# Performance work log

Measured on AMD Instinct MI355X. Metric: run time of the kernel, lower is better.

The kernel has to match this reference:

```python
import jax, jax.numpy as jnp
import numpy as np

B, N, F_IN, F_OUT = 65536, 17, 64, 64


def setup_inputs() -> dict:
    key = jax.random.key(0)
    k1, k2, k3, k4 = jax.random.split(key, 4)
    x = jax.random.normal(k1, (B, N, F_IN), dtype=jnp.float32)
    adj = jax.random.uniform(k2, (N, N), dtype=jnp.float32)
    # symmetric 0/1-ish skeleton adjacency with self structure kept dense as in the module
    adj = (adj + adj.T) * 0.5
    weight_self = jax.random.normal(k3, (F_IN, F_OUT), dtype=jnp.float32) * (1.0 / np.sqrt(F_IN))
    weight_neighbor = jax.random.normal(k4, (F_IN, F_OUT), dtype=jnp.float32) * (1.0 / np.sqrt(F_IN))
    bias = jnp.zeros((F_OUT,), dtype=jnp.float32)
    return {"x": x, "adj": adj, "weight_self": weight_self,
            "weight_neighbor": weight_neighbor, "bias": bias}


def reference(x, adj, weight_self, weight_neighbor, bias):
    # out_self[b,n,o] = x[b,n,i] * W_self[i,o]
    out_self = jnp.einsum('bni,io->bno', x, weight_self)
    # neighbor aggregation: adj[n,m] * x[b,m,i]
    x_neighbors = jnp.einsum('nm,bmi->bni', adj, x)
    out_neighbors = jnp.einsum('bni,io->bno', x_neighbors, weight_neighbor)
    return out_self + out_neighbors + bias
```

## Files before the change

kernel.cpp:

```cpp
#include <hip/hip_runtime.h>
#include <stdint.h>

#define NNODE  17
#define FDIM   64
#define NBLOCK 512
#define GPW    32
#define SROW   68
#define WSTR   132

typedef __attribute__((ext_vector_type(4)))  short short4v;
typedef __attribute__((ext_vector_type(8)))  short short8v;
typedef __attribute__((ext_vector_type(16))) float f32x16;

__device__ __forceinline__ uint32_t bf16b(float f) {
    uint32_t u = __float_as_uint(f);
    return (u + 0x7fffu + ((u >> 16) & 1u)) >> 16;
}
__device__ __forceinline__ uint32_t bfpack(float lo, float hi) {
    return bf16b(lo) | (bf16b(hi) << 16);
}
__device__ __forceinline__ short8v ld8(const uint16_t* p) {
    short4v lo = *(const short4v*)p;
    short4v hi = *(const short4v*)(p + 4);
    return __builtin_shufflevector(lo, hi, 0, 1, 2, 3, 4, 5, 6, 7);
}
__device__ __forceinline__ short8v mk8(uint32_t w0, uint32_t w1, uint32_t w2, uint32_t w3) {
    union { uint32_t u[4]; short8v v; } c;
    c.u[0] = w0; c.u[1] = w1; c.u[2] = w2; c.u[3] = w3;
    return c.v;
}

__global__ __launch_bounds__(256, 2) void egc_kernel(
    const float* __restrict__ x, const float* __restrict__ adj,
    const float* __restrict__ wself, const float* __restrict__ wneigh,
    const float* __restrict__ bias, float* __restrict__ out)
{
    __shared__ uint16_t sMem[4 * 32 * SROW];
    __shared__ float sAdj[NNODE * NNODE];
    __shared__ float sBias[FDIM];

    const int t  = threadIdx.x;
    const int l  = t & 63;
    const int wv = t >> 6;
    const int n_ = l & 31;
    const int h_ = l >> 5;

    const int    gw    = blockIdx.x * 4 + wv;
    const size_t gbase = (size_t)gw * GPW;

    const float4* xg = (const float4*)x + gbase * 272;
    float4 pf0, pf1, pf2, pf3, pf4;
    pf0 = xg[l]; pf1 = xg[l + 64]; pf2 = xg[l + 128]; pf3 = xg[l + 192];
    if (l < 16) pf4 = xg[256 + l];

    for (int idx = t; idx < FDIM * 128; idx += 256) {
        int o = idx >> 7, k = idx & 127;
        float v = (k < 64) ? wself[k * 64 + o] : wneigh[(k - 64) * 64 + o];
        sMem[o * WSTR + k] = (uint16_t)bf16b(v);
    }
    for (int i = t; i < NNODE * NNODE; i += 256) sAdj[i] = adj[i];
    if (t < FDIM) sBias[t] = bias[t];
    __syncthreads();

    short8v wS[2][4], wN[2][4];
    #pragma unroll
    for (int nt = 0; nt < 2; ++nt)
        #pragma unroll
        for (int ks = 0; ks < 4; ++ks) {
            wS[nt][ks] = ld8(&sMem[(32 * nt + n_) * WSTR + 16 * ks + 8 * h_]);
            wN[nt][ks] = ld8(&sMem[(32 * nt + n_) * WSTR + 64 + 16 * ks + 8 * h_]);
        }
    const float bias0 = sBias[n_], bias1 = sBias[32 + n_];

    short8v adjA[2];
    #pragma unroll
    for (int ks = 0; ks < 2; ++ks) {
        short8v v;
        #pragma unroll
        for (int e = 0; e < 8; ++e) {
            int k = 16 * ks + 8 * h_ + e;
            float a = (n_ < NNODE && k < NNODE) ? sAdj[n_ * NNODE + k] : 0.f;
            v[e] = (short)bf16b(a);
        }
        adjA[ks] = v;
    }
    __syncthreads();
    for (int i = t; i < 4 * 32 * SROW; i += 256) sMem[i] = 0;
    __syncthreads();

    uint16_t* strip = &sMem[wv * 32 * SROW];
    float* outg = out + gbase * (size_t)(NNODE * FDIM);

    for (int g = 0; g < GPW; ++g) {
        {
            uint2 pk; int idx, row, c4;
            idx = l;       row = idx >> 4; c4 = (idx & 15) << 2;
            pk.x = bfpack(pf0.x, pf0.y); pk.y = bfpack(pf0.z, pf0.w);
            *(uint2*)&strip[row * SROW + c4] = pk;
            idx = l + 64;  row = idx >> 4; c4 = (idx & 15) << 2;
            pk.x = bfpack(pf1.x, pf1.y); pk.y = bfpack(pf1.z, pf1.w);
            *(uint2*)&strip[row * SROW + c4] = pk;
            idx = l + 128; row = idx >> 4; c4 = (idx & 15) << 2;
            pk.x = bfpack(pf2.x, pf2.y); pk.y = bfpack(pf2.z, pf2.w);
            *(uint2*)&strip[row * SROW + c4] = pk;
            idx = l + 192; row = idx >> 4; c4 = (idx & 15) << 2;
            pk.x = bfpack(pf3.x, pf3.y); pk.y = bfpack(pf3.z, pf3.w);
            *(uint2*)&strip[row * SROW + c4] = pk;
            if (l < 16) {
                pk.x = bfpack(pf4.x, pf4.y); pk.y = bfpack(pf4.z, pf4.w);
                *(uint2*)&strip[16 * SROW + (l << 2)] = pk;
            }
        }
        if (g + 1 < GPW) {
            xg += 272;
            pf0 = xg[l]; pf1 = xg[l + 64]; pf2 = xg[l + 128]; pf3 = xg[l + 192];
            if (l < 16) pf4 = xg[256 + l];
        }

        short8v a0 = ld8(&strip[n_ * SROW + 0  + 8 * h_]);
        short8v a1 = ld8(&strip[n_ * SROW + 16 + 8 * h_]);
        short8v a2 = ld8(&strip[n_ * SROW + 32 + 8 * h_]);
        short8v a3 = ld8(&strip[n_ * SROW + 48 + 8 * h_]);

        f32x16 s0, s1, h0, h1;
        #pragma unroll
        for (int r = 0; r < 16; ++r) { s0[r] = bias0; s1[r] = bias1; h0[r] = 0.f; h1[r] = 0.f; }

        s0 = __builtin_amdgcn_mfma_f32_32x32x16_bf16(a0, wS[0][0], s0, 0, 0, 0);
        s1 = __builtin_amdgcn_mfma_f32_32x32x16_bf16(a0, wS[1][0], s1, 0, 0, 0);
        h0 = __builtin_amdgcn_mfma_f32_32x32x16_bf16(a0, wN[0][0], h0, 0, 0, 0);
        h1 = __builtin_amdgcn_mfma_f32_32x32x16_bf16(a0, wN[1][0], h1, 0, 0, 0);
        s0 = __builtin_amdgcn_mfma_f32_32x32x16_bf16(a1, wS[0][1], s0, 0, 0, 0);
        s1 = __builtin_amdgcn_mfma_f32_32x32x16_bf16(a1, wS[1][1], s1, 0, 0, 0);
        h0 = __builtin_amdgcn_mfma_f32_32x32x16_bf16(a1, wN[0][1], h0, 0, 0, 0);
        h1 = __builtin_amdgcn_mfma_f32_32x32x16_bf16(a1, wN[1][1], h1, 0, 0, 0);
        s0 = __builtin_amdgcn_mfma_f32_32x32x16_bf16(a2, wS[0][2], s0, 0, 0, 0);
        s1 = __builtin_amdgcn_mfma_f32_32x32x16_bf16(a2, wS[1][2], s1, 0, 0, 0);
        h0 = __builtin_amdgcn_mfma_f32_32x32x16_bf16(a2, wN[0][2], h0, 0, 0, 0);
        h1 = __builtin_amdgcn_mfma_f32_32x32x16_bf16(a2, wN[1][2], h1, 0, 0, 0);
        s0 = __builtin_amdgcn_mfma_f32_32x32x16_bf16(a3, wS[0][3], s0, 0, 0, 0);
        s1 = __builtin_amdgcn_mfma_f32_32x32x16_bf16(a3, wS[1][3], s1, 0, 0, 0);
        h0 = __builtin_amdgcn_mfma_f32_32x32x16_bf16(a3, wN[0][3], h0, 0, 0, 0);
        h1 = __builtin_amdgcn_mfma_f32_32x32x16_bf16(a3, wN[1][3], h1, 0, 0, 0);

        #define HB_ADJ(SACC, HACC)                                                        \
        {                                                                                  \
            _Pragma("unroll")                                                              \
            for (int ks2 = 0; ks2 < 2; ++ks2) {                                            \
                const int rb = 8 * ks2;                                                    \
                float o0_ = __shfl_xor(h_ ? HACC[rb + 0] : HACC[rb + 4], 32);              \
                float o1_ = __shfl_xor(h_ ? HACC[rb + 1] : HACC[rb + 5], 32);              \
                float o2_ = __shfl_xor(h_ ? HACC[rb + 2] : HACC[rb + 6], 32);              \
                float o3_ = __shfl_xor(h_ ? HACC[rb + 3] : HACC[rb + 7], 32);              \
                uint32_t l01 = bfpack(HACC[rb + 0], HACC[rb + 1]);                         \
                uint32_t l23 = bfpack(HACC[rb + 2], HACC[rb + 3]);                         \
                uint32_t l45 = bfpack(HACC[rb + 4], HACC[rb + 5]);                         \
                uint32_t l67 = bfpack(HACC[rb + 6], HACC[rb + 7]);                         \
                uint32_t o01 = bfpack(o0_, o1_);                                           \
                uint32_t o23 = bfpack(o2_, o3_);                                           \
                uint32_t w0 = h_ ? o01 : l01;                                              \
                uint32_t w1 = h_ ? o23 : l23;                                              \
                uint32_t w2 = h_ ? l45 : o01;                                              \
                uint32_t w3 = h_ ? l67 : o23;                                              \
                SACC = __builtin_amdgcn_mfma_f32_32x32x16_bf16(                            \
                    adjA[ks2], mk8(w0, w1, w2, w3), SACC, 0, 0, 0);                        \
            }                                                                              \
        }
        HB_ADJ(s0, h0)
        HB_ADJ(s1, h1)
        #undef HB_ADJ

        {
            float* og = outg + (size_t)g * (NNODE * FDIM);
            #pragma unroll
            for (int r = 0; r < 9; ++r) {
                int row = (r & 3) + 8 * (r >> 2) + 4 * h_;
                if (row < NNODE) {
                    og[row * 64 + n_]      = s0[r];
                    og[row * 64 + 32 + n_] = s1[r];
                }
            }
        }
    }
}

extern "C" void kernel_launch(void* const* d_in, const int* in_sizes, int n_in,
                              void* d_out, int out_size, void* d_ws, size_t ws_size,
                              hipStream_t stream) {
    (void)in_sizes; (void)n_in; (void)d_ws; (void)ws_size; (void)out_size;
    const float* x      = (const float*)d_in[0];
    const float* adj    = (const float*)d_in[1];
    const float* wself  = (const float*)d_in[2];
    const float* wneigh = (const float*)d_in[3];
    const float* bias   = (const float*)d_in[4];
    float* out = (float*)d_out;
    egc_kernel<<<NBLOCK, 256, 0, stream>>>(x, adj, wself, wneigh, bias, out);
}
```

Measured before the change: 136.5 us.

## Use hardware bf16 pack and permlane32 swap, double grid with higher occupancy

After: 277.6 us. 103% more time.

```diff
diff --git a/kernel.cpp b/kernel.cpp
--- a/kernel.cpp
+++ b/kernel.cpp
@@ -1,10 +1,11 @@
 #include <hip/hip_runtime.h>
+#include <hip/hip_bf16.h>
 #include <stdint.h>
 
 #define NNODE  17
 #define FDIM   64
-#define NBLOCK 512
-#define GPW    32
+#define NBLOCK 1024
+#define GPW    16
 #define SROW   68
 #define WSTR   132
 
@@ -16,8 +17,9 @@
     uint32_t u = __float_as_uint(f);
     return (u + 0x7fffu + ((u >> 16) & 1u)) >> 16;
 }
-__device__ __forceinline__ uint32_t bfpack(float lo, float hi) {
-    return bf16b(lo) | (bf16b(hi) << 16);
+__device__ __forceinline__ uint32_t cvtpk(float lo, float hi) {
+    __hip_bfloat162 b = __float22bfloat162_rn(make_float2(lo, hi));
+    return *reinterpret_cast<uint32_t*>(&b);
 }
 __device__ __forceinline__ short8v ld8(const uint16_t* p) {
     short4v lo = *(const short4v*)p;
@@ -30,7 +32,7 @@
     return c.v;
 }
 
-__global__ __launch_bounds__(256, 2) void egc_kernel(
+__global__ __launch_bounds__(256, 3) void egc_kernel(
     const float* __restrict__ x, const float* __restrict__ adj,
     const float* __restrict__ wself, const float* __restrict__ wneigh,
     const float* __restrict__ bias, float* __restrict__ out)
@@ -95,19 +97,19 @@
         {
             uint2 pk; int idx, row, c4;
             idx = l;       row = idx >> 4; c4 = (idx & 15) << 2;
-            pk.x = bfpack(pf0.x, pf0.y); pk.y = bfpack(pf0.z, pf0.w);
+            pk.x = cvtpk(pf0.x, pf0.y); pk.y = cvtpk(pf0.z, pf0.w);
             *(uint2*)&strip[row * SROW + c4] = pk;
             idx = l + 64;  row = idx >> 4; c4 = (idx & 15) << 2;
-            pk.x = bfpack(pf1.x, pf1.y); pk.y = bfpack(pf1.z, pf1.w);
+            pk.x = cvtpk(pf1.x, pf1.y); pk.y = cvtpk(pf1.z, pf1.w);
             *(uint2*)&strip[row * SROW + c4] = pk;
             idx = l + 128; row = idx >> 4; c4 = (idx & 15) << 2;
-            pk.x = bfpack(pf2.x, pf2.y); pk.y = bfpack(pf2.z, pf2.w);
+            pk.x = cvtpk(pf2.x, pf2.y); pk.y = cvtpk(pf2.z, pf2.w);
             *(uint2*)&strip[row * SROW + c4] = pk;
             idx = l + 192; row = idx >> 4; c4 = (idx & 15) << 2;
-            pk.x = bfpack(pf3.x, pf3.y); pk.y = bfpack(pf3.z, pf3.w);
+            pk.x = cvtpk(pf3.x, pf3.y); pk.y = cvtpk(pf3.z, pf3.w);
             *(uint2*)&strip[row * SROW + c4] = pk;
             if (l < 16) {
-                pk.x = bfpack(pf4.x, pf4.y); pk.y = bfpack(pf4.z, pf4.w);
+                pk.x = cvtpk(pf4.x, pf4.y); pk.y = cvtpk(pf4.z, pf4.w);
                 *(uint2*)&strip[16 * SROW + (l << 2)] = pk;
             }
         }
@@ -148,22 +150,14 @@
             _Pragma("unroll")                                                              \
             for (int ks2 = 0; ks2 < 2; ++ks2) {                                            \
                 const int rb = 8 * ks2;                                                    \
-                float o0_ = __shfl_xor(h_ ? HACC[rb + 0] : HACC[rb + 4], 32);              \
-                float o1_ = __shfl_xor(h_ ? HACC[rb + 1] : HACC[rb + 5], 32);              \
-                float o2_ = __shfl_xor(h_ ? HACC[rb + 2] : HACC[rb + 6], 32);              \
-                float o3_ = __shfl_xor(h_ ? HACC[rb + 3] : HACC[rb + 7], 32);              \
-                uint32_t l01 = bfpack(HACC[rb + 0], HACC[rb + 1]);                         \
-                uint32_t l23 = bfpack(HACC[rb + 2], HACC[rb + 3]);                         \
-                uint32_t l45 = bfpack(HACC[rb + 4], HACC[rb + 5]);                         \
-                uint32_t l67 = bfpack(HACC[rb + 6], HACC[rb + 7]);                         \
-                uint32_t o01 = bfpack(o0_, o1_);                                           \
-                uint32_t o23 = bfpack(o2_, o3_);                                           \
-                uint32_t w0 = h_ ? o01 : l01;                                              \
-                uint32_t w1 = h_ ? o23 : l23;                                              \
-                uint32_t w2 = h_ ? l45 : o01;                                              \
-                uint32_t w3 = h_ ? l67 : o23;                                              \
+                uint32_t A01 = cvtpk(HACC[rb + 0], HACC[rb + 1]);                          \
+                uint32_t C23 = cvtpk(HACC[rb + 2], HACC[rb + 3]);                          \
+                uint32_t B45 = cvtpk(HACC[rb + 4], HACC[rb + 5]);                          \
+                uint32_t D67 = cvtpk(HACC[rb + 6], HACC[rb + 7]);                          \
+                asm("v_permlane32_swap_b32 %0, %1" : "+v"(A01), "+v"(B45));                \
+                asm("v_permlane32_swap_b32 %0, %1" : "+v"(C23), "+v"(D67));                \
                 SACC = __builtin_amdgcn_mfma_f32_32x32x16_bf16(                            \
-                    adjA[ks2], mk8(w0, w1, w2, w3), SACC, 0, 0, 0);                        \
+                    adjA[ks2], mk8(A01, C23, B45, D67), SACC, 0, 0, 0);                    \
             }                                                                              \
         }
         HB_ADJ(s0, h0)
```
